# Optimization experiments

Hardware: AMD Instinct MI355X
Metric: run time of the kernel (lower is better)

Reference implementation:

```python
import jax, jax.numpy as jnp
import numpy as np

B, L, DIM = 16, 4096, 512
N_FFT, HOP, WIN = 1024, 256, 1024
PAD = (WIN - HOP) // 2  # 'same' padding trim
OUT_DIM = N_FFT + 2


def hann_window(win):
    n = jnp.arange(win, dtype=jnp.float32)
    return 0.5 - 0.5 * jnp.cos(2.0 * jnp.pi * n / win)


def setup_inputs() -> dict:
    key = jax.random.key(0)
    k1, k2 = jax.random.split(key)
    x = jax.random.normal(k1, (B, L, DIM), dtype=jnp.float32)
    W = jax.random.normal(k2, (OUT_DIM, DIM), dtype=jnp.float32) * 0.02
    b = jnp.zeros((OUT_DIM,), dtype=jnp.float32)
    return {"x": x, "W": W, "b": b}


def _istft(S):
    # S: (B, N_FFT//2+1, T) complex rfft spectrum
    T = S.shape[-1]
    frames = jnp.fft.irfft(S, n=N_FFT, axis=1)
    window = hann_window(WIN)
    frames = frames * window[None, :, None]
    out_len = (T - 1) * HOP + WIN
    idx = jnp.arange(T)[:, None] * HOP + jnp.arange(WIN)[None, :]
    fr = frames.transpose(0, 2, 1)
    y = jnp.zeros((fr.shape[0], out_len), fr.dtype).at[:, idx].add(fr)
    env = jnp.zeros((out_len,), fr.dtype).at[idx].add(
        jnp.broadcast_to(window * window, idx.shape))
    y = y[:, PAD:out_len - PAD]
    env = env[PAD:out_len - PAD]
    return y / env


def reference(x, W, b):
    # Linear projection: (B, L, DIM) -> (B, L, N_FFT+2)
    h = jnp.einsum('bld,od->blo', x, W) + b
    h = h.transpose(0, 2, 1)                              # (B, N_FFT+2, L)
    mag, p = jnp.split(h, 2, axis=1)                      # each (B, N_FFT//2+1, L)
    mag = jnp.minimum(jnp.exp(mag), 100.0)                # exp + clip(max=100)
    S = mag * jax.lax.complex(jnp.cos(p), jnp.sin(p))
    return _istft(S)                                      # (B, L*HOP)
```

## Files before the change

kernel.cpp:

```cpp
#include <hip/hip_runtime.h>
#include <hip/hip_bf16.h>
#include <math.h>

#define BATCH   16
#define TFRM    4096
#define DIM     512
#define NFFT    1024
#define HOP     256
#define PADC    384
#define MROWS   (BATCH*TFRM)
#define OUTLEN  1048576
#define TWO_PI_OVER_N 0.006135923151542565f
#define INV_TWO_PI    0.15915494309189535f
#define EPS0    148
#define EPS1    68

typedef __bf16 bf16x8 __attribute__((ext_vector_type(8)));
typedef float  f32x16 __attribute__((ext_vector_type(16)));

__device__ __forceinline__ ushort f2bf(float f) {
  union { float f; unsigned u; } v; v.f = f;
  unsigned u = v.u;
  unsigned r = (u + 0x7FFFu + ((u >> 16) & 1u)) >> 16;
  return (ushort)r;
}
__device__ __forceinline__ float bf2f(ushort h) {
  union { unsigned u; float f; } v; v.u = ((unsigned)h) << 16;
  return v.f;
}
__device__ __forceinline__ float fast_sin(float x) { return __builtin_amdgcn_sinf(x * INV_TWO_PI); }
__device__ __forceinline__ float fast_cos(float x) { return __builtin_amdgcn_cosf(x * INV_TWO_PI); }
__device__ __forceinline__ float fast_exp(float x) { return __builtin_amdgcn_exp2f(x * 1.4426950408889634f); }
__device__ __forceinline__ float dpp_xor1(float v) {
  return __int_as_float(__builtin_amdgcn_update_dpp(
      __float_as_int(v), __float_as_int(v), 0xB1, 0xF, 0xF, false));
}

__global__ void k_prep_x(const float* __restrict__ x, const float* __restrict__ W,
                         const float* __restrict__ bias,
                         ushort* __restrict__ xbf, float* __restrict__ s512) {
  const int row  = blockIdx.x * 4 + (threadIdx.x >> 6);
  const int lane = threadIdx.x & 63;
  const float* xr = x + (size_t)row * DIM + lane * 8;
  float4 v0 = *(const float4*)xr;
  float4 v1 = *(const float4*)(xr + 4);
  ushort4 u0, u1;
  u0.x = f2bf(v0.x); u0.y = f2bf(v0.y); u0.z = f2bf(v0.z); u0.w = f2bf(v0.w);
  u1.x = f2bf(v1.x); u1.y = f2bf(v1.y); u1.z = f2bf(v1.z); u1.w = f2bf(v1.w);
  ushort* xo = xbf + (size_t)row * DIM + lane * 8;
  *(ushort4*)xo = u0;
  *(ushort4*)(xo + 4) = u1;
  const float* w0 = W + 512 * DIM + lane * 8;
  const float* w1 = W + 1025 * DIM + lane * 8;
  float4 a0 = *(const float4*)w0, a1 = *(const float4*)(w0 + 4);
  float4 b0 = *(const float4*)w1, b1 = *(const float4*)(w1 + 4);
  float sm = v0.x*a0.x + v0.y*a0.y + v0.z*a0.z + v0.w*a0.w
           + v1.x*a1.x + v1.y*a1.y + v1.z*a1.z + v1.w*a1.w;
  float sp = v0.x*b0.x + v0.y*b0.y + v0.z*b0.z + v0.w*b0.w
           + v1.x*b1.x + v1.y*b1.y + v1.z*b1.z + v1.w*b1.w;
#pragma unroll
  for (int off = 32; off; off >>= 1) {
    sm += __shfl_down(sm, off);
    sp += __shfl_down(sp, off);
  }
  if (lane == 0) {
    float mag = fminf(fast_exp(sm + bias[512]), 100.0f);
    s512[row] = mag * fast_cos(sp + bias[1025]) * (1.0f / 1024.0f);
  }
}

__global__ void k_prep_w(const float* __restrict__ W, ushort* __restrict__ o) {
  int i = blockIdx.x * 256 + threadIdx.x;
  int r = i >> 9;
  int c = i & 511;
  int orig = (r >> 1) + (r & 1) * 513;
  o[i] = f2bf(W[orig * DIM + c]);
}

__global__ void k_basis(ushort* __restrict__ basE, ushort* __restrict__ basO) {
  int r = blockIdx.x;
  int n = r + 1;
  for (int k = threadIdx.x; k < 512; k += 256) {
    float e, o;
    if (k == 0) { e = 1.0f / 1024.0f; o = 0.0f; }
    else {
      int ph = (k * n) & 1023;
      float ang = (float)ph * TWO_PI_OVER_N;
      e = 2.0f * cosf(ang) * (1.0f / 1024.0f);
      o = 2.0f * sinf(ang) * (1.0f / 1024.0f);
    }
    basE[r * 512 + k] = f2bf(e);
    basO[r * 512 + k] = f2bf(o);
  }
}

template<int EPI>
__global__ __launch_bounds__(256) void k_gemm(const ushort* A, const ushort* A2, int lda,
                                              const ushort* Bt, const ushort* Bt2, int ldb,
                                              ushort* C, ushort* C2, int ldc,
                                              int nbn, int NK, int nsplit,
                                              const float* __restrict__ bias,
                                              const float* __restrict__ s512) {
  __shared__ __align__(16) ushort lds[3][2][128 * 32];
  const int tid  = threadIdx.x;
  const int cpx  = gridDim.x >> 3;
  int bid  = (blockIdx.x & 7) * cpx + (blockIdx.x >> 3);
  bool second = false;
  if (nsplit > 0 && bid >= nsplit) { second = true; A = A2; Bt = Bt2; C = C2; bid -= nsplit; }
  const int bm   = bid / nbn;
  const int bn   = bid - bm * nbn;
  const int lane = tid & 63;
  const int wv   = tid >> 6;
  const int wr   = (wv >> 1) * 64;
  const int wc   = (wv & 1) * 64;
  const int l31  = lane & 31;
  const int kh   = lane >> 5;
  const int rsw  = (lane >> 1) & 3;

  f32x16 acc[2][2] = {};

  const int swz = ((tid & 3) ^ ((tid >> 3) & 3)) << 3;
  auto stage = [&](const ushort* __restrict__ g, int ld, int row0, int k0, ushort* l) {
#pragma unroll
    for (int p = 0; p < 2; ++p) {
      int i = tid + p * 256;
      const ushort* gp = g + (size_t)(row0 + (i >> 2)) * ld + k0 + swz;
      ushort* lp = l + ((i >> 6) << 9);
      __builtin_amdgcn_global_load_lds(
          (const __attribute__((address_space(1))) void*)gp,
          (__attribute__((address_space(3))) void*)lp, 16, 0, 0);
    }
  };
  auto frag = [&](const ushort* lb, int rowbase, int ks) -> bf16x8 {
    const int row = rowbase + l31;
    return *(const bf16x8*)(lb + row * 32 + (((ks * 2 + kh) ^ rsw) << 3));
  };

  stage(A,  lda, bm * 128, 0,  &lds[0][0][0]);
  stage(Bt, ldb, bn * 128, 0,  &lds[0][1][0]);
  stage(A,  lda, bm * 128, 32, &lds[1][0][0]);
  stage(Bt, ldb, bn * 128, 32, &lds[1][1][0]);
  asm volatile("s_waitcnt vmcnt(4)" ::: "memory");
  __syncthreads();

  int sl = 0;
  for (int t = 0; t < NK; ++t) {
    if (t + 2 < NK) {
      const int psl = (sl >= 1) ? sl - 1 : 2;
      stage(A,  lda, bm * 128, (t + 2) << 5, &lds[psl][0][0]);
      stage(Bt, ldb, bn * 128, (t + 2) << 5, &lds[psl][1][0]);
    }
    const ushort* lA = &lds[sl][0][0];
    const ushort* lB = &lds[sl][1][0];
    bf16x8 aF[2][2], bF[2][2];
#pragma unroll
    for (int ks = 0; ks < 2; ++ks) {
#pragma unroll
      for (int m = 0; m < 2; ++m) aF[ks][m] = frag(lA, wr + m * 32, ks);
#pragma unroll
      for (int n = 0; n < 2; ++n) bF[ks][n] = frag(lB, wc + n * 32, ks);
    }
#pragma unroll
    for (int ks = 0; ks < 2; ++ks)
#pragma unroll
      for (int m = 0; m < 2; ++m)
#pragma unroll
        for (int n = 0; n < 2; ++n)
          acc[m][n] = __builtin_amdgcn_mfma_f32_32x32x16_bf16(aF[ks][m], bF[ks][n],
                                                              acc[m][n], 0, 0, 0);
    if (t + 2 < NK)      asm volatile("s_waitcnt vmcnt(4)" ::: "memory");
    else if (t + 2 == NK) asm volatile("s_waitcnt vmcnt(0)" ::: "memory");
    if (t + 1 < NK) __syncthreads();
    sl = (sl >= 2) ? 0 : sl + 1;
  }

  ushort* epi = &lds[0][0][0];
  const bool odd = lane & 1;
  __syncthreads();

  if constexpr (EPI == 0) {
#pragma unroll
    for (int m = 0; m < 2; ++m) {
#pragma unroll
      for (int q = 0; q < 4; ++q) {
        const int lrow0 = wr + m * 32 + q * 8 + (kh << 2);
        float4 sv4 = {0.f, 0.f, 0.f, 0.f};
        if (!second) sv4 = *(const float4*)(s512 + bm * 128 + lrow0);
#pragma unroll
        for (int rr = 0; rr < 4; ++rr) {
          const float sv = ((const float*)&sv4)[rr];
          const float par = second ? 0.0f : (odd ? sv : -sv);
          const int lrow = lrow0 + rr;
#pragma unroll
          for (int n = 0; n < 2; ++n) {
            const int c = wc + n * 32 + l31;
            epi[lrow * EPS0 + c] = f2bf(acc[m][n][q * 4 + rr] + par);
          }
        }
      }
    }
    __syncthreads();
#pragma unroll
    for (int i = 0; i < 8; ++i) {
      int row = (tid >> 4) + i * 16;
      int co  = (tid & 15) << 3;
      bf16x8 v = *(const bf16x8*)(epi + row * EPS0 + co);
      *(bf16x8*)(C + (size_t)(bm * 128 + row) * ldc + bn * 128 + co) = v;
    }
  } else {
    ushort* tA = epi;
    ushort* tB = epi + 128 * EPS1;
#pragma unroll
    for (int n = 0; n < 2; ++n) {
      const int cl  = wc + n * 32 + l31;
      const int kk  = (bn * 128 + cl) >> 1;
      const float bs = bias[odd ? 513 + kk : kk];
      ushort* dst = (odd ? tB : tA);
      const int kkl = cl >> 1;
#pragma unroll
      for (int m = 0; m < 2; ++m)
#pragma unroll
        for (int q = 0; q < 4; ++q)
#pragma unroll
          for (int rr = 0; rr < 4; ++rr) {
            const int lrow = wr + m * 32 + q * 8 + (kh << 2) + rr;
            float v = acc[m][n][q * 4 + rr] + bs;
            float pv = dpp_xor1(v);
            float hm = odd ? pv : v;
            float hp = odd ? v : pv;
            float mag = fminf(fast_exp(hm), 100.0f);
            float outv = odd ? mag * fast_sin(hp) : mag * fast_cos(hp);
            dst[lrow * EPS1 + kkl] = f2bf(outv);
          }
    }
    __syncthreads();
#pragma unroll
    for (int i = 0; i < 4; ++i) {
      int row = (tid >> 3) + i * 32;
      int co  = (tid & 7) << 3;
      size_t go = (size_t)(bm * 128 + row) * ldc + bn * 64 + co;
      bf16x8 va = *(const bf16x8*)(tA + row * EPS1 + co);
      *(bf16x8*)(C + go) = va;
      bf16x8 vb = *(const bf16x8*)(tB + row * EPS1 + co);
      *(bf16x8*)(C2 + go) = vb;
    }
  }
}

__global__ void k_oa(const ushort* __restrict__ E, const ushort* __restrict__ O,
                     float* __restrict__ out) {
  int u = blockIdx.x * 256 + threadIdx.x;
  int b  = u >> 18;
  int g  = u & 262143;
  int s  = (g << 2) + PADC;
  int t0 = s >> 8;
  int nb = s & 255;
  float acc[4] = {0.f, 0.f, 0.f, 0.f};
  bool interior = (t0 >= 3) && (t0 < TFRM);
  float env[4];
#pragma unroll
  for (int j = 0; j < 4; ++j) env[j] = interior ? 1.5f : 0.0f;
#pragma unroll
  for (int q = 0; q < 4; ++q) {
    int t = t0 - q;
    if (t < 0 || t >= TFRM) continue;
    int n = nb + (q << 8);
    size_t base = ((size_t)(b << 12) + t) << 9;
    float w[4];
#pragma unroll
    for (int j = 0; j < 4; ++j) {
      w[j] = 0.5f - 0.5f * __builtin_amdgcn_cosf((float)(n + j) * (1.0f / 1024.0f));
      if (!interior) env[j] += w[j] * w[j];
    }
    float d[4];
    if (n <= 508) {
      ushort4 e1 = *(const ushort4*)(E + base + n);
      ushort4 o1 = *(const ushort4*)(O + base + n);
      if (n >= 4) {
        ushort4 e0 = *(const ushort4*)(E + base + n - 4);
        ushort4 o0 = *(const ushort4*)(O + base + n - 4);
        d[0] = bf2f(e0.w) - bf2f(o0.w);
      } else d[0] = 0.0f;
      d[1] = bf2f(e1.x) - bf2f(o1.x);
      d[2] = bf2f(e1.y) - bf2f(o1.y);
      d[3] = bf2f(e1.z) - bf2f(o1.z);
    } else if (n == 512) {
      ushort4 e = *(const ushort4*)(E + base + 508);
      ushort4 o = *(const ushort4*)(O + base + 508);
      d[0] = bf2f(e.w) - bf2f(o.w);
      d[1] = bf2f(e.z) + bf2f(o.z);
      d[2] = bf2f(e.y) + bf2f(o.y);
      d[3] = bf2f(e.x) + bf2f(o.x);
    } else {
      ushort4 e = *(const ushort4*)(E + base + 1020 - n);
      ushort4 o = *(const ushort4*)(O + base + 1020 - n);
      d[0] = bf2f(e.w) + bf2f(o.w);
      d[1] = bf2f(e.z) + bf2f(o.z);
      d[2] = bf2f(e.y) + bf2f(o.y);
      d[3] = bf2f(e.x) + bf2f(o.x);
    }
#pragma unroll
    for (int j = 0; j < 4; ++j) acc[j] += w[j] * d[j];
  }
  float4 o4;
  o4.x = acc[0] / env[0]; o4.y = acc[1] / env[1];
  o4.z = acc[2] / env[2]; o4.w = acc[3] / env[3];
  *(float4*)(out + (size_t)u * 4) = o4;
}

extern "C" void kernel_launch(void* const* d_in, const int* in_sizes, int n_in,
                              void* d_out, int out_size, void* d_ws, size_t ws_size,
                              hipStream_t stream) {
  const float* x    = (const float*)d_in[0];
  const float* W    = (const float*)d_in[1];
  const float* bias = (const float*)d_in[2];
  float* out = (float*)d_out;
  char* ws = (char*)d_ws;

  ushort* xbf  = (ushort*)(ws + 0);
  ushort* Epp  = (ushort*)(ws + 0);
  ushort* h_a  = (ushort*)(ws + 67108864);
  ushort* h_b  = (ushort*)(ws + 134217728);
  ushort* Obuf = (ushort*)(ws + 201326592);
  ushort* Wp   = (ushort*)(ws + 268435456);
  ushort* basE = (ushort*)(ws + 269484032);
  ushort* basO = (ushort*)(ws + 270008320);
  float*  s512 = (float*) (ws + 270532608);

  k_prep_x<<<MROWS / 4, 256, 0, stream>>>(x, W, bias, xbf, s512);
  k_prep_w<<<(1024 * 512) / 256, 256, 0, stream>>>(W, Wp);
  k_basis<<<512, 256, 0, stream>>>(basE, basO);

  k_gemm<1><<<(MROWS / 128) * 8, 256, 0, stream>>>(
      xbf, nullptr, DIM, Wp, nullptr, DIM, h_a, h_b, 512, 8, 16, 0, bias, nullptr);

  k_gemm<0><<<2 * (MROWS / 128) * 4, 256, 0, stream>>>(
      h_a, h_b, 512, basE, basO, 512, Epp, Obuf, 512, 4, 16, (MROWS / 128) * 4,
      nullptr, s512);

  k_oa<<<(BATCH * OUTLEN) / 1024, 256, 0, stream>>>(Epp, Obuf, out);
}
```

Baseline: 312.9 us.

## Store intermediates in MFMA fragment order and run LDS-free second GEMM

The first GEMM now writes h_a/h_b, and the basis kernel writes basE/basO, directly in a per-lane MFMA fragment-packed layout. The second GEMM becomes a new kernel where each wave owns a 64x64 tile and loads fragments straight from global memory with register double-buffering, skipping LDS staging and block barriers. This removes LDS traffic and __syncthreads from the inverse-DFT GEMM. In exchange, each wave re-reads its operands from global or L2 memory without sharing them through LDS, and the code relies on hand-placed waitcnt and sched_barrier instructions.

```diff
diff --git a/kernel.cpp b/kernel.cpp
--- a/kernel.cpp
+++ b/kernel.cpp
@@ -12,7 +12,6 @@
 #define OUTLEN  1048576
 #define TWO_PI_OVER_N 0.006135923151542565f
 #define INV_TWO_PI    0.15915494309189535f
-#define EPS0    148
 #define EPS1    68
 
 typedef __bf16 bf16x8 __attribute__((ext_vector_type(8)));
@@ -34,6 +33,9 @@
 __device__ __forceinline__ float dpp_xor1(float v) {
   return __int_as_float(__builtin_amdgcn_update_dpp(
       __float_as_int(v), __float_as_int(v), 0xB1, 0xF, 0xF, false));
+}
+__device__ __forceinline__ f32x16 MF(bf16x8 a, bf16x8 b, f32x16 c) {
+  return __builtin_amdgcn_mfma_f32_32x32x16_bf16(a, b, c, 0, 0, 0);
 }
 
 __global__ void k_prep_x(const float* __restrict__ x, const float* __restrict__ W,
@@ -78,35 +80,36 @@
 }
 
 __global__ void k_basis(ushort* __restrict__ basE, ushort* __restrict__ basO) {
-  int r = blockIdx.x;
-  int n = r + 1;
-  for (int k = threadIdx.x; k < 512; k += 256) {
-    float e, o;
-    if (k == 0) { e = 1.0f / 1024.0f; o = 0.0f; }
-    else {
-      int ph = (k * n) & 1023;
-      float ang = (float)ph * TWO_PI_OVER_N;
-      e = 2.0f * cosf(ang) * (1.0f / 1024.0f);
-      o = 2.0f * sinf(ang) * (1.0f / 1024.0f);
-    }
-    basE[r * 512 + k] = f2bf(e);
-    basO[r * 512 + k] = f2bf(o);
-  }
-}
-
-template<int EPI>
-__global__ __launch_bounds__(256) void k_gemm(const ushort* A, const ushort* A2, int lda,
-                                              const ushort* Bt, const ushort* Bt2, int ldb,
-                                              ushort* C, ushort* C2, int ldc,
-                                              int nbn, int NK, int nsplit,
-                                              const float* __restrict__ bias,
-                                              const float* __restrict__ s512) {
+  int i = blockIdx.x * 256 + threadIdx.x;
+  int j    = i & 7;
+  int lane = (i >> 3) & 63;
+  int ft   = i >> 9;
+  int t    = ft & 31;
+  int rg   = ft >> 5;
+  int r    = rg * 32 + (lane & 31);
+  int k    = t * 16 + ((lane >> 5) << 3) + j;
+  int n    = r + 1;
+  float e, o;
+  if (k == 0) { e = 1.0f / 1024.0f; o = 0.0f; }
+  else {
+    int ph = (k * n) & 1023;
+    float ang = (float)ph * TWO_PI_OVER_N;
+    e = 2.0f * cosf(ang) * (1.0f / 1024.0f);
+    o = 2.0f * sinf(ang) * (1.0f / 1024.0f);
+  }
+  basE[i] = f2bf(e);
+  basO[i] = f2bf(o);
+}
+
+__global__ __launch_bounds__(256) void k_gemm1(const ushort* __restrict__ A, int lda,
+                                               const ushort* __restrict__ Bt, int ldb,
+                                               ushort* __restrict__ Ca, ushort* __restrict__ Cb,
+                                               int nbn, int NK,
+                                               const float* __restrict__ bias) {
   __shared__ __align__(16) ushort lds[3][2][128 * 32];
   const int tid  = threadIdx.x;
   const int cpx  = gridDim.x >> 3;
-  int bid  = (blockIdx.x & 7) * cpx + (blockIdx.x >> 3);
-  bool second = false;
-  if (nsplit > 0 && bid >= nsplit) { second = true; A = A2; Bt = Bt2; C = C2; bid -= nsplit; }
+  const int bid  = ((int)blockIdx.x & 7) * cpx + ((int)blockIdx.x >> 3);
   const int bm   = bid / nbn;
   const int bn   = bid - bm * nbn;
   const int lane = tid & 63;
@@ -166,8 +169,7 @@
       for (int m = 0; m < 2; ++m)
 #pragma unroll
         for (int n = 0; n < 2; ++n)
-          acc[m][n] = __builtin_amdgcn_mfma_f32_32x32x16_bf16(aF[ks][m], bF[ks][n],
-                                                              acc[m][n], 0, 0, 0);
+          acc[m][n] = MF(aF[ks][m], bF[ks][n], acc[m][n]);
     if (t + 2 < NK)      asm volatile("s_waitcnt vmcnt(4)" ::: "memory");
     else if (t + 2 == NK) asm volatile("s_waitcnt vmcnt(0)" ::: "memory");
     if (t + 1 < NK) __syncthreads();
@@ -175,76 +177,132 @@
   }
 
   ushort* epi = &lds[0][0][0];
+  ushort* tA = epi;
+  ushort* tB = epi + 128 * EPS1;
   const bool odd = lane & 1;
   __syncthreads();
-
-  if constexpr (EPI == 0) {
-#pragma unroll
-    for (int m = 0; m < 2; ++m) {
-#pragma unroll
-      for (int q = 0; q < 4; ++q) {
-        const int lrow0 = wr + m * 32 + q * 8 + (kh << 2);
-        float4 sv4 = {0.f, 0.f, 0.f, 0.f};
-        if (!second) sv4 = *(const float4*)(s512 + bm * 128 + lrow0);
+#pragma unroll
+  for (int n = 0; n < 2; ++n) {
+    const int cl  = wc + n * 32 + l31;
+    const int kk  = (bn * 128 + cl) >> 1;
+    const float bs = bias[odd ? 513 + kk : kk];
+    ushort* dst = (odd ? tB : tA);
+    const int kkl = cl >> 1;
+#pragma unroll
+    for (int m = 0; m < 2; ++m)
+#pragma unroll
+      for (int q = 0; q < 4; ++q)
 #pragma unroll
         for (int rr = 0; rr < 4; ++rr) {
-          const float sv = ((const float*)&sv4)[rr];
-          const float par = second ? 0.0f : (odd ? sv : -sv);
-          const int lrow = lrow0 + rr;
-#pragma unroll
-          for (int n = 0; n < 2; ++n) {
-            const int c = wc + n * 32 + l31;
-            epi[lrow * EPS0 + c] = f2bf(acc[m][n][q * 4 + rr] + par);
-          }
+          const int lrow = wr + m * 32 + q * 8 + (kh << 2) + rr;
+          float v = acc[m][n][q * 4 + rr] + bs;
+          float pv = dpp_xor1(v);
+          float hm = odd ? pv : v;
+          float hp = odd ? v : pv;
+          float mag = fminf(fast_exp(hm), 100.0f);
+          float outv = odd ? mag * fast_sin(hp) : mag * fast_cos(hp);
+          dst[lrow * EPS1 + kkl] = f2bf(outv);
         }
+  }
+  __syncthreads();
+  const int tl = tid >> 6;
+  const int l  = tid & 63;
+#pragma unroll
+  for (int it = 0; it < 4; ++it) {
+    const int row = it * 32 + (l & 31);
+    const int kl  = tl * 16 + ((l >> 5) << 3);
+    size_t go = (((size_t)(bm * 4 + it) * 32 + bn * 4 + tl) * 64 + l) * 8;
+    *(bf16x8*)(Ca + go) = *(const bf16x8*)(tA + row * EPS1 + kl);
+    *(bf16x8*)(Cb + go) = *(const bf16x8*)(tB + row * EPS1 + kl);
+  }
+}
+
+__global__ __launch_bounds__(256) void k_gemm2(const ushort* __restrict__ hA,
+                                               const ushort* __restrict__ hB,
+                                               const ushort* __restrict__ basE,
+                                               const ushort* __restrict__ basO,
+                                               ushort* __restrict__ E, ushort* __restrict__ O,
+                                               const float* __restrict__ s512) {
+  __shared__ __align__(16) ushort lds[4][64 * 72];
+  const int tid  = threadIdx.x;
+  const int cpx  = gridDim.x >> 3;
+  const int bid  = ((int)blockIdx.x & 7) * cpx + ((int)blockIdx.x >> 3);
+  const int wv   = tid >> 6;
+  const int lane = tid & 63;
+  const int wid  = bid * 4 + wv;
+  const bool isO = wid >= 8192;
+  const int w    = wid & 8191;
+  const int mt   = w >> 3;
+  const int nt   = w & 7;
+  const ushort* A  = isO ? hB : hA;
+  const ushort* B  = isO ? basO : basE;
+  ushort* Cp = isO ? O : E;
+
+  const ushort* pa0 = A + (((size_t)(mt * 2) * 32) * 64 + lane) * 8;
+  const ushort* pa1 = pa0 + (size_t)32 * 64 * 8;
+  const ushort* pb0 = B + (((size_t)(nt * 2) * 32) * 64 + lane) * 8;
+  const ushort* pb1 = pb0 + (size_t)32 * 64 * 8;
+
+  f32x16 acc[2][2] = {};
+  bf16x8 aE0, aE1, bE0, bE1, aO0, aO1, bO0, bO1;
+
+#define LDG2(dst, ptr) asm volatile("global_load_dwordx4 %0, %1, off" : "=v"(dst) : "v"(ptr))
+#define LOADSET_E(toff) { LDG2(aE0, pa0 + (toff) * 512); LDG2(aE1, pa1 + (toff) * 512); \
+                          LDG2(bE0, pb0 + (toff) * 512); LDG2(bE1, pb1 + (toff) * 512); }
+#define LOADSET_O(toff) { LDG2(aO0, pa0 + (toff) * 512); LDG2(aO1, pa1 + (toff) * 512); \
+                          LDG2(bO0, pb0 + (toff) * 512); LDG2(bO1, pb1 + (toff) * 512); }
+
+  LOADSET_E(0);
+  LOADSET_O(1);
+  asm volatile("s_waitcnt vmcnt(4)" ::: "memory");
+  __builtin_amdgcn_sched_barrier(0);
+
+#pragma unroll
+  for (int t = 0; t < 32; t += 2) {
+    acc[0][0] = MF(aE0, bE0, acc[0][0]); acc[0][1] = MF(aE0, bE1, acc[0][1]);
+    acc[1][0] = MF(aE1, bE0, acc[1][0]); acc[1][1] = MF(aE1, bE1, acc[1][1]);
+    if (t + 2 < 32) { LOADSET_E(t + 2); asm volatile("s_waitcnt vmcnt(4)" ::: "memory"); }
+    else            { asm volatile("s_waitcnt vmcnt(0)" ::: "memory"); }
+    __builtin_amdgcn_sched_barrier(0);
+    acc[0][0] = MF(aO0, bO0, acc[0][0]); acc[0][1] = MF(aO0, bO1, acc[0][1]);
+    acc[1][0] = MF(aO1, bO0, acc[1][0]); acc[1][1] = MF(aO1, bO1, acc[1][1]);
+    if (t + 2 < 32) {
+      LOADSET_O(t + 3);
+      asm volatile("s_waitcnt vmcnt(4)" ::: "memory");
+      __builtin_amdgcn_sched_barrier(0);
+    }
+  }
+
+  ushort* wl = &lds[wv][0];
+  const int kh  = lane >> 5;
+  const int l31 = lane & 31;
+  const bool odd = lane & 1;
+#pragma unroll
+  for (int m = 0; m < 2; ++m)
+#pragma unroll
+    for (int q = 0; q < 4; ++q) {
+      const int rowb = m * 32 + q * 8 + (kh << 2);
+      float4 sv4 = {0.f, 0.f, 0.f, 0.f};
+      if (!isO) sv4 = *(const float4*)(s512 + mt * 64 + rowb);
+#pragma unroll
+      for (int rr = 0; rr < 4; ++rr) {
+        const float sv = ((const float*)&sv4)[rr];
+        const float par = isO ? 0.0f : (odd ? sv : -sv);
+#pragma unroll
+        for (int n = 0; n < 2; ++n)
+          wl[(rowb + rr) * 72 + n * 32 + l31] = f2bf(acc[m][n][q * 4 + rr] + par);
       }
     }
-    __syncthreads();
-#pragma unroll
-    for (int i = 0; i < 8; ++i) {
-      int row = (tid >> 4) + i * 16;
-      int co  = (tid & 15) << 3;
-      bf16x8 v = *(const bf16x8*)(epi + row * EPS0 + co);
-      *(bf16x8*)(C + (size_t)(bm * 128 + row) * ldc + bn * 128 + co) = v;
-    }
-  } else {
-    ushort* tA = epi;
-    ushort* tB = epi + 128 * EPS1;
-#pragma unroll
-    for (int n = 0; n < 2; ++n) {
-      const int cl  = wc + n * 32 + l31;
-      const int kk  = (bn * 128 + cl) >> 1;
-      const float bs = bias[odd ? 513 + kk : kk];
-      ushort* dst = (odd ? tB : tA);
-      const int kkl = cl >> 1;
-#pragma unroll
-      for (int m = 0; m < 2; ++m)
-#pragma unroll
-        for (int q = 0; q < 4; ++q)
-#pragma unroll
-          for (int rr = 0; rr < 4; ++rr) {
-            const int lrow = wr + m * 32 + q * 8 + (kh << 2) + rr;
-            float v = acc[m][n][q * 4 + rr] + bs;
-            float pv = dpp_xor1(v);
-            float hm = odd ? pv : v;
-            float hp = odd ? v : pv;
-            float mag = fminf(fast_exp(hm), 100.0f);
-            float outv = odd ? mag * fast_sin(hp) : mag * fast_cos(hp);
-            dst[lrow * EPS1 + kkl] = f2bf(outv);
-          }
-    }
-    __syncthreads();
-#pragma unroll
-    for (int i = 0; i < 4; ++i) {
-      int row = (tid >> 3) + i * 32;
-      int co  = (tid & 7) << 3;
-      size_t go = (size_t)(bm * 128 + row) * ldc + bn * 64 + co;
-      bf16x8 va = *(const bf16x8*)(tA + row * EPS1 + co);
-      *(bf16x8*)(C + go) = va;
-      bf16x8 vb = *(const bf16x8*)(tB + row * EPS1 + co);
-      *(bf16x8*)(C2 + go) = vb;
-    }
-  }
+#pragma unroll
+  for (int it = 0; it < 8; ++it) {
+    const int lrow = (lane >> 3) + it * 8;
+    const int lcol = (lane & 7) << 3;
+    bf16x8 v = *(const bf16x8*)(wl + lrow * 72 + lcol);
+    *(bf16x8*)(Cp + ((size_t)(mt * 64 + lrow) << 9) + nt * 64 + lcol) = v;
+  }
+#undef LDG2
+#undef LOADSET_E
+#undef LOADSET_O
 }
 
 __global__ void k_oa(const ushort* __restrict__ E, const ushort* __restrict__ O,
@@ -329,14 +387,11 @@
 
   k_prep_x<<<MROWS / 4, 256, 0, stream>>>(x, W, bias, xbf, s512);
   k_prep_w<<<(1024 * 512) / 256, 256, 0, stream>>>(W, Wp);
-  k_basis<<<512, 256, 0, stream>>>(basE, basO);
-
-  k_gemm<1><<<(MROWS / 128) * 8, 256, 0, stream>>>(
-      xbf, nullptr, DIM, Wp, nullptr, DIM, h_a, h_b, 512, 8, 16, 0, bias, nullptr);
-
-  k_gemm<0><<<2 * (MROWS / 128) * 4, 256, 0, stream>>>(
-      h_a, h_b, 512, basE, basO, 512, Epp, Obuf, 512, 4, 16, (MROWS / 128) * 4,
-      nullptr, s512);
+  k_basis<<<(512 * 512) / 256, 256, 0, stream>>>(basE, basO);
+
+  k_gemm1<<<(MROWS / 128) * 8, 256, 0, stream>>>(xbf, DIM, Wp, DIM, h_a, h_b, 8, 16, bias);
+
+  k_gemm2<<<4096, 256, 0, stream>>>(h_a, h_b, basE, basO, Epp, Obuf, s512);
 
   k_oa<<<(BATCH * OUTLEN) / 1024, 256, 0, stream>>>(Epp, Obuf, out);
 }
```

New measurement: 304.0 us. 1.03x faster.
